# Kernel tuning notes

Measured on AMD Instinct MI355X. Metric: run time of the kernel, lower is better.

Reference implementation:

```python
import jax, jax.numpy as jnp
import numpy as np

L = 2048      # atoms
I = 512       # tokens (tok_idx.max()+1, fixed for jit)
C_ATOM = 128
C_PAIR = 16
C_TOK = 384
F1D = 3 + 1 + 128 + 256  # concat of atom 1d features = 388
NB, NH, HD = 3, 4, 32    # atom transformer blocks / heads / head dim
FF = 4 * C_ATOM


def _w(k, shape, fan_in):
    return jax.random.normal(k, shape, jnp.float32) / np.sqrt(fan_in)


def setup_inputs() -> dict:
    key = jax.random.key(0)
    ks = jax.random.split(key, 32)
    inp = {
        'ref_pos': jax.random.normal(ks[0], (L, 3), jnp.float32),
        'ref_charge': jax.random.normal(ks[1], (L, 1), jnp.float32),
        'ref_element': jax.random.uniform(ks[2], (L, 128), jnp.float32),
        'ref_atom_name_chars': jax.random.uniform(ks[3], (L, 256), jnp.float32),
        'ref_space_uid': jnp.sort(jax.random.randint(ks[4], (L,), 0, 64, jnp.int32)),
        'atom_to_token_map': jnp.sort(jax.random.randint(ks[5], (L,), 0, I, jnp.int32)),
        # linearNoBias weights stored (in, out)
        'W_in': _w(ks[6], (F1D, C_ATOM), F1D),
        'W_d': _w(ks[7], (3, C_PAIR), 3),
        'W_invd': _w(ks[8], (1, C_PAIR), 1),
        'W_vm': _w(ks[9], (1, C_PAIR), 1),
        'W_sl': _w(ks[10], (C_ATOM, C_PAIR), C_ATOM),
        'W_sm': _w(ks[11], (C_ATOM, C_PAIR), C_ATOM),
        'Wp1': _w(ks[12], (C_PAIR, C_PAIR), C_PAIR),
        'Wp2': _w(ks[13], (C_PAIR, C_PAIR), C_PAIR),
        'Wp3': _w(ks[14], (C_PAIR, C_PAIR), C_PAIR),
        'Wq_tok': _w(ks[15], (C_ATOM, C_TOK), C_ATOM),
        # atom transformer (stacked over NB blocks)
        'Wq': _w(ks[16], (NB, C_ATOM, C_ATOM), C_ATOM),
        'Wk': _w(ks[17], (NB, C_ATOM, C_ATOM), C_ATOM),
        'Wv': _w(ks[18], (NB, C_ATOM, C_ATOM), C_ATOM),
        'Wb': _w(ks[19], (NB, C_PAIR, NH), C_PAIR),
        'Wo': _w(ks[20], (NB, C_ATOM, C_ATOM), C_ATOM),
        'Wt1': _w(ks[21], (NB, C_ATOM, FF), C_ATOM),
        'Wt2': _w(ks[22], (NB, FF, C_ATOM), FF),
    }
    return inp


def _ln(x):
    mu = jnp.mean(x, axis=-1, keepdims=True)
    var = jnp.mean(jnp.square(x - mu), axis=-1, keepdims=True)
    return (x - mu) * jax.lax.rsqrt(var + 1e-5)


def _forward(ref_pos, ref_charge, ref_element, ref_atom_name_chars,
             ref_space_uid, atom_to_token_map,
             W_in, W_d, W_invd, W_vm, W_sl, W_sm, Wp1, Wp2, Wp3, Wq_tok,
             Wq, Wk, Wv, Wb, Wo, Wt1, Wt2):
    relu = jax.nn.relu
    # C_L: [L, c_atom]
    feat = jnp.concatenate([ref_pos, ref_charge, ref_element, ref_atom_name_chars], axis=-1)
    C_L = feat @ W_in
    # pairwise geometry: D_LL [L, L, 3], valid mask V_LL [L, L, 1]
    D = ref_pos[:, None, :] - ref_pos[None, :, :]
    Vf = (ref_space_uid[:, None] == ref_space_uid[None, :]).astype(C_L.dtype)[..., None]
    P = (D @ W_d) * Vf
    inv_d = 1.0 / (1.0 + jnp.linalg.norm(D, axis=-1, keepdims=True))
    P = P + (inv_d @ W_invd) * Vf
    P = P + (Vf @ W_vm) * Vf
    P = P + (relu(C_L) @ W_sl)[:, None, :] + (relu(C_L) @ W_sm)[None, :, :]
    P = P + relu(relu(relu(P) @ Wp1) @ Wp2) @ Wp3  # pair_mlp residual
    # atom transformer with pair bias
    Q = C_L
    scale = 1.0 / np.sqrt(HD)
    for b in range(NB):
        x = _ln(Q)
        q = (x @ Wq[b]).reshape(L, NH, HD)
        k = (x @ Wk[b]).reshape(L, NH, HD)
        v = (x @ Wv[b]).reshape(L, NH, HD)
        bias = P @ Wb[b]                                   # [L, L, NH]
        logits = jnp.einsum('lhd,mhd->lmh', q, k) * scale + bias
        a = jax.nn.softmax(logits, axis=1)                 # over keys m
        o = jnp.einsum('lmh,mhd->lhd', a, v).reshape(L, C_ATOM)
        Q = Q + o @ Wo[b]
        y = _ln(Q)
        Q = Q + relu(y @ Wt1[b]) @ Wt2[b]
    # process_q then scatter-mean (index_reduce 'mean', include_self=False)
    pQ = relu(Q @ Wq_tok)                                  # [L, c_token]
    tok = atom_to_token_map
    sums = jax.ops.segment_sum(pQ, tok, num_segments=I)
    cnt = jax.ops.segment_sum(jnp.ones((L, 1), pQ.dtype), tok, num_segments=I)
    A_I = sums / jnp.maximum(cnt, 1.0)
    return A_I, Q, C_L, P


def reference(ref_pos, ref_charge, ref_element, ref_atom_name_chars,
              ref_space_uid, atom_to_token_map,
              W_in, W_d, W_invd, W_vm, W_sl, W_sm, Wp1, Wp2, Wp3, Wq_tok,
              Wq, Wk, Wv, Wb, Wo, Wt1, Wt2):
    return _forward(ref_pos, ref_charge, ref_element, ref_atom_name_chars,
                    ref_space_uid, atom_to_token_map,
                    W_in, W_d, W_invd, W_vm, W_sl, W_sm, Wp1, Wp2, Wp3, Wq_tok,
                    Wq, Wk, Wv, Wb, Wo, Wt1, Wt2)
```

## Files before the change

kernel.cpp:

```cpp
#include <hip/hip_runtime.h>
#include <hip/hip_bf16.h>
#include <hip/hip_fp16.h>

#define L_ATOMS 2048
#define N_TOK 512
#define CA 128
#define CP 16
#define CT 384
#define NBLK 3
#define NHEAD 4
#define HDIM 32
#define FFD 512
#define F1D 388

typedef _Float16 half8 __attribute__((ext_vector_type(8)));
typedef _Float16 half4_t __attribute__((ext_vector_type(4)));
typedef float f32x4 __attribute__((ext_vector_type(4)));

__global__ __launch_bounds__(256) void k_cl(
    const float* __restrict__ pos, const float* __restrict__ charge,
    const float* __restrict__ elem, const float* __restrict__ chars,
    const float* __restrict__ W_in, const float* __restrict__ W_sl,
    const float* __restrict__ W_sm,
    float* __restrict__ out_cl, float* __restrict__ out_q,
    float* __restrict__ csl, float* __restrict__ csm) {
  __shared__ float feat_s[4][F1D];
  __shared__ float rcl_s[4][CA];
  const int t = threadIdx.x;
  const int l0 = blockIdx.x * 4;
  if (t < 12) feat_s[t / 3][t % 3] = pos[l0 * 3 + t];
  else if (t < 16) feat_s[t - 12][3] = charge[l0 + t - 12];
  for (int k = 0; k < 2; k++) {
    int idx = t + k * 256;
    feat_s[idx >> 7][4 + (idx & 127)] = elem[l0 * 128 + idx];
  }
  for (int k = 0; k < 4; k++) {
    int idx = t + k * 256;
    feat_s[idx >> 8][132 + (idx & 255)] = chars[l0 * 256 + idx];
  }
  __syncthreads();
  const int c = t & 127, rh = t >> 7;
  float acc[2] = {0.f, 0.f};
  for (int f4 = 0; f4 < F1D; f4 += 4) {
    float w0 = W_in[(f4 + 0) * CA + c];
    float w1 = W_in[(f4 + 1) * CA + c];
    float w2 = W_in[(f4 + 2) * CA + c];
    float w3 = W_in[(f4 + 3) * CA + c];
#pragma unroll
    for (int r = 0; r < 2; r++) {
      float4 fv = *(const float4*)&feat_s[rh * 2 + r][f4];
      acc[r] += fv.x * w0 + fv.y * w1 + fv.z * w2 + fv.w * w3;
    }
  }
#pragma unroll
  for (int r = 0; r < 2; r++) {
    int l = l0 + rh * 2 + r;
    out_cl[l * CA + c] = acc[r];
    out_q[l * CA + c] = acc[r];
    rcl_s[rh * 2 + r][c] = fmaxf(acc[r], 0.f);
  }
  __syncthreads();
  if (t < 128) {
    const int r = t >> 5, j = t & 15, mat = (t >> 4) & 1;
    const float* W = mat ? W_sm : W_sl;
    float a = 0.f;
    for (int i4 = 0; i4 < CA; i4 += 4) {
      float4 xv = *(const float4*)&rcl_s[r][i4];
      a += xv.x * W[i4 * CP + j] + xv.y * W[(i4 + 1) * CP + j] +
           xv.z * W[(i4 + 2) * CP + j] + xv.w * W[(i4 + 3) * CP + j];
    }
    float* dst = mat ? csm : csl;
    dst[(l0 + r) * CP + j] = a;
  }
}

__global__ __launch_bounds__(256, 4) void k_pair(
    const float* __restrict__ pos, const int* __restrict__ uid,
    const float* __restrict__ csl, const float* __restrict__ csm,
    const float* __restrict__ W_d, const float* __restrict__ W_invd,
    const float* __restrict__ W_vm, const float* __restrict__ Wp1,
    const float* __restrict__ Wp2, const float* __restrict__ Wp3,
    const float* __restrict__ Wb,
    float* __restrict__ P_out, _Float16* __restrict__ bias_hp, int use_bias) {
  __shared__ _Float16 bias_lds[12 * 2 * 256];
  const int t = threadIdx.x;
  const int w = t >> 6, lane = t & 63;
  const int q = lane >> 4, j16 = lane & 15;
  const int c4 = q * 4;
  const int m_base = blockIdx.x * 256;
  const int l0 = blockIdx.y * 2;
  half4_t w1f, w2f, w3f, wbf;
#pragma unroll
  for (int r = 0; r < 4; r++) {
    w1f[r] = (_Float16)Wp1[(c4 + r) * 16 + j16];
    w2f[r] = (_Float16)Wp2[(c4 + r) * 16 + j16];
    w3f[r] = (_Float16)Wp3[(c4 + r) * 16 + j16];
  }
  if (j16 < 12) {
    int bb = j16 >> 2, hh = j16 & 3;
#pragma unroll
    for (int r = 0; r < 4; r++)
      wbf[r] = (_Float16)Wb[(bb * 16 + c4 + r) * 4 + hh];
  } else {
    wbf = half4_t{0, 0, 0, 0};
  }
  const float4 wdx = *(const float4*)(W_d + c4);
  const float4 wdy = *(const float4*)(W_d + 16 + c4);
  const float4 wdz = *(const float4*)(W_d + 32 + c4);
  const float4 wiv = *(const float4*)(W_invd + c4);
  const float4 wvm = *(const float4*)(W_vm + c4);
  const float4 cl[2] = {*(const float4*)(csl + l0 * 16 + c4),
                        *(const float4*)(csl + (l0 + 1) * 16 + c4)};
  const float plx[2] = {pos[l0 * 3 + 0], pos[(l0 + 1) * 3 + 0]};
  const float ply[2] = {pos[l0 * 3 + 1], pos[(l0 + 1) * 3 + 1]};
  const float plz[2] = {pos[l0 * 3 + 2], pos[(l0 + 1) * 3 + 2]};
  const int uidl[2] = {uid[l0], uid[l0 + 1]};
  const f32x4 z = {0.f, 0.f, 0.f, 0.f};
#pragma unroll
  for (int it = 0; it < 4; it++) {
    const int moff = w * 64 + it * 16 + j16;
    const int m = m_base + moff;
    const float pmx = pos[m * 3 + 0], pmy = pos[m * 3 + 1],
                pmz = pos[m * 3 + 2];
    const int um = uid[m];
    const float4 cm = *(const float4*)(csm + m * 16 + c4);
#pragma unroll
    for (int li = 0; li < 2; li++) {
      const int lg = l0 + li;
      float dx = plx[li] - pmx, dy = ply[li] - pmy, dz = plz[li] - pmz;
      float vfm = (uidl[li] == um) ? 1.f : 0.f;
      float d2 = dx * dx + dy * dy + dz * dz;
      float invd_v =
          vfm * __builtin_amdgcn_rcpf(1.f + __builtin_amdgcn_sqrtf(d2));
      float dxv = dx * vfm, dyv = dy * vfm, dzv = dz * vfm;
      float pv[4];
      pv[0] = dxv * wdx.x + dyv * wdy.x + dzv * wdz.x + invd_v * wiv.x +
              vfm * wvm.x + cl[li].x + cm.x;
      pv[1] = dxv * wdx.y + dyv * wdy.y + dzv * wdz.y + invd_v * wiv.y +
              vfm * wvm.y + cl[li].y + cm.y;
      pv[2] = dxv * wdx.z + dyv * wdy.z + dzv * wdz.z + invd_v * wiv.z +
              vfm * wvm.z + cl[li].z + cm.z;
      pv[3] = dxv * wdx.w + dyv * wdy.w + dzv * wdz.w + invd_v * wiv.w +
              vfm * wvm.w + cl[li].w + cm.w;
      half4_t b0, b1, b2;
#pragma unroll
      for (int r = 0; r < 4; r++) b0[r] = (_Float16)fmaxf(pv[r], 0.f);
      f32x4 d = __builtin_amdgcn_mfma_f32_16x16x16f16(w1f, b0, z, 0, 0, 0);
#pragma unroll
      for (int r = 0; r < 4; r++) b1[r] = (_Float16)fmaxf(d[r], 0.f);
      d = __builtin_amdgcn_mfma_f32_16x16x16f16(w2f, b1, z, 0, 0, 0);
#pragma unroll
      for (int r = 0; r < 4; r++) b2[r] = (_Float16)fmaxf(d[r], 0.f);
      d = __builtin_amdgcn_mfma_f32_16x16x16f16(w3f, b2, z, 0, 0, 0);
      float pf[4];
#pragma unroll
      for (int r = 0; r < 4; r++) pf[r] = pv[r] + d[r];
      *(float4*)(P_out + ((size_t)lg * L_ATOMS + m) * 16 + c4) =
          make_float4(pf[0], pf[1], pf[2], pf[3]);
      if (use_bias) {
        half4_t bf;
#pragma unroll
        for (int r = 0; r < 4; r++) bf[r] = (_Float16)pf[r];
        f32x4 db = __builtin_amdgcn_mfma_f32_16x16x16f16(wbf, bf, z, 0, 0, 0);
        if (q < 3) {
#pragma unroll
          for (int r = 0; r < 4; r++)
            bias_lds[((q * 4 + r) * 2 + li) * 256 + moff] = (_Float16)db[r];
        }
      }
    }
  }
  if (use_bias) {
    __syncthreads();
    const size_t plane = (size_t)L_ATOMS * L_ATOMS;
#pragma unroll
    for (int kk = 0; kk < 3; kk++) {
      int cid = t + kk * 256;
      int pl = cid >> 6;
      int lrow = (cid >> 5) & 1;
      int chunk = cid & 31;
      half8 v = *(const half8*)&bias_lds[(pl * 2 + lrow) * 256 + chunk * 8];
      *(half8*)(bias_hp + pl * plane + (size_t)(l0 + lrow) * L_ATOMS + m_base +
                chunk * 8) = v;
    }
  }
}

__global__ __launch_bounds__(512, 4) void k_lnqkv(
    const float* __restrict__ Qg, const float* __restrict__ Wq,
    const float* __restrict__ Wk, const float* __restrict__ Wv,
    _Float16* __restrict__ q_hd, _Float16* __restrict__ k_hd,
    _Float16* __restrict__ vT_hd) {
  __shared__ float x_s[4][CA];
  const int t = threadIdx.x;
  const int l0 = blockIdx.x * 4;
  if (t < 128) ((float4*)x_s)[t] = ((const float4*)(Qg + l0 * CA))[t];
  __syncthreads();
  if (t < 128) {
    const int r = t >> 5, i = t & 31;
    float s1 = 0.f, s2 = 0.f;
#pragma unroll
    for (int k = 0; k < 4; k++) {
      float x = x_s[r][i + 32 * k];
      s1 += x;
      s2 += x * x;
    }
#pragma unroll
    for (int m = 1; m <= 16; m <<= 1) {
      s1 += __shfl_xor(s1, m);
      s2 += __shfl_xor(s2, m);
    }
    float mu = s1 * (1.f / 128.f);
    float var = s2 * (1.f / 128.f) - mu * mu;
    float inv = 1.f / sqrtf(var + 1e-5f);
#pragma unroll
    for (int k = 0; k < 4; k++)
      x_s[r][i + 32 * k] = (x_s[r][i + 32 * k] - mu) * inv;
  }
  __syncthreads();
  const int c = t & 127, rh = t >> 7;
  const int h = c >> 5, d = c & 31;
  const int l = l0 + rh;
#pragma unroll
  for (int mat = 0; mat < 3; mat++) {
    const float* W = mat == 0 ? Wq : (mat == 1 ? Wk : Wv);
    float acc = 0.f;
    for (int i4 = 0; i4 < CA; i4 += 4) {
      float w0 = W[(i4 + 0) * CA + c];
      float w1 = W[(i4 + 1) * CA + c];
      float w2 = W[(i4 + 2) * CA + c];
      float w3 = W[(i4 + 3) * CA + c];
      float4 xv = *(const float4*)&x_s[rh][i4];
      acc += xv.x * w0 + xv.y * w1 + xv.z * w2 + xv.w * w3;
    }
    if (mat == 0)
      q_hd[(h * L_ATOMS + l) * HDIM + d] = (_Float16)acc;
    else if (mat == 1)
      k_hd[(h * L_ATOMS + l) * HDIM + d] = (_Float16)acc;
    else
      vT_hd[(h * HDIM + d) * L_ATOMS + l] = (_Float16)acc;
  }
}

template <int USE_BIAS>
__global__ __launch_bounds__(512, 4) void k_attn(
    const _Float16* __restrict__ q_hd, const _Float16* __restrict__ k_hd,
    const _Float16* __restrict__ vT_hd, const _Float16* __restrict__ bias_hp,
    const float* __restrict__ Pmat, const float* __restrict__ Wb,
    float* __restrict__ o_buf, int b) {
  __shared__ __align__(16) _Float16 p_lds[8][16][40];
  __shared__ float o_sh[8][16][33];
  __shared__ float M_sh[8][16];
  __shared__ float S_sh[8][16];
  __shared__ float wb_s[16];
  const int t = threadIdx.x;
  const int w = t >> 6, lane = t & 63;
  const int l0 = blockIdx.x * 16;
  const int h = blockIdx.y;
  if (USE_BIAS == 0) {
    if (t < 16) wb_s[t] = Wb[(b * 16 + t) * 4 + h];
    __syncthreads();
  }
  const int c16 = lane & 15, q4 = lane >> 4;
  half8 qa = *(const half8*)(q_hd + ((h * L_ATOMS + l0 + c16) * HDIM + q4 * 8));
  f32x4 o0 = {0.f, 0.f, 0.f, 0.f}, o1 = {0.f, 0.f, 0.f, 0.f};
  float M = -INFINITY;
  float S = 0.f;
  const float scale = 0.17677669529663687f;
  const _Float16* bias_row =
      bias_hp + ((size_t)(b * 4 + h) * L_ATOMS + (l0 + c16)) * L_ATOMS;
  for (int it = 0; it < 8; it++) {
    const int m0 = w * 256 + it * 32;
    half8 kb0 =
        *(const half8*)(k_hd + ((h * L_ATOMS + m0 + c16) * HDIM + q4 * 8));
    half8 kb1 =
        *(const half8*)(k_hd + ((h * L_ATOMS + m0 + 16 + c16) * HDIM + q4 * 8));
    half8 vb0 =
        *(const half8*)(vT_hd + ((h * HDIM + c16) * L_ATOMS + m0 + q4 * 8));
    half8 vb1 = *(const half8*)(vT_hd +
                                ((h * HDIM + 16 + c16) * L_ATOMS + m0 + q4 * 8));
    f32x4 z = {0.f, 0.f, 0.f, 0.f};
    f32x4 c0 = __builtin_amdgcn_mfma_f32_16x16x32_f16(kb0, qa, z, 0, 0, 0);
    f32x4 c1 = __builtin_amdgcn_mfma_f32_16x16x32_f16(kb1, qa, z, 0, 0, 0);
    float l0v[4], l1v[4];
    if (USE_BIAS) {
      half4_t bh0 = *(const half4_t*)(bias_row + m0 + q4 * 4);
      half4_t bh1 = *(const half4_t*)(bias_row + m0 + 16 + q4 * 4);
#pragma unroll
      for (int r = 0; r < 4; r++) {
        l0v[r] = c0[r] * scale + (float)bh0[r];
        l1v[r] = c1[r] * scale + (float)bh1[r];
      }
    } else {
#pragma unroll
      for (int r = 0; r < 4; r++) {
        const float* Pp0 =
            Pmat + ((size_t)(l0 + c16) * L_ATOMS + m0 + q4 * 4 + r) * 16;
        const float* Pp1 = Pp0 + 16 * 16;
        float a0 = 0.f, a1 = 0.f;
#pragma unroll
        for (int c2 = 0; c2 < 16; c2++) {
          a0 += Pp0[c2] * wb_s[c2];
          a1 += Pp1[c2] * wb_s[c2];
        }
        l0v[r] = c0[r] * scale + a0;
        l1v[r] = c1[r] * scale + a1;
      }
    }
    float tm = fmaxf(fmaxf(fmaxf(l0v[0], l0v[1]), fmaxf(l0v[2], l0v[3])),
                     fmaxf(fmaxf(l1v[0], l1v[1]), fmaxf(l1v[2], l1v[3])));
    tm = fmaxf(tm, __shfl_xor(tm, 16));
    tm = fmaxf(tm, __shfl_xor(tm, 32));
    float Mn = fmaxf(M, tm);
    float al = __expf(M - Mn);
    float p0[4], p1[4], ps = 0.f;
#pragma unroll
    for (int r = 0; r < 4; r++) {
      p0[r] = __expf(l0v[r] - Mn);
      p1[r] = __expf(l1v[r] - Mn);
      ps += p0[r] + p1[r];
    }
    float rs = ps + __shfl_xor(ps, 16);
    rs += __shfl_xor(rs, 32);
    S = S * al + rs;
    M = Mn;
    half4_t ph0, ph1;
#pragma unroll
    for (int r = 0; r < 4; r++) {
      ph0[r] = (_Float16)p0[r];
      ph1[r] = (_Float16)p1[r];
    }
    *(half4_t*)&p_lds[w][c16][q4 * 4] = ph0;
    *(half4_t*)&p_lds[w][c16][16 + q4 * 4] = ph1;
    float alr[4];
#pragma unroll
    for (int r = 0; r < 4; r++) alr[r] = __shfl(al, q4 * 4 + r);
#pragma unroll
    for (int r = 0; r < 4; r++) {
      o0[r] *= alr[r];
      o1[r] *= alr[r];
    }
    asm volatile("" ::: "memory");
    __builtin_amdgcn_sched_barrier(0);
    half8 pa = *(const half8*)(&p_lds[w][c16][q4 * 8]);
    o0 = __builtin_amdgcn_mfma_f32_16x16x32_f16(pa, vb0, o0, 0, 0, 0);
    o1 = __builtin_amdgcn_mfma_f32_16x16x32_f16(pa, vb1, o1, 0, 0, 0);
    asm volatile("" ::: "memory");
    __builtin_amdgcn_sched_barrier(0);
  }
#pragma unroll
  for (int r = 0; r < 4; r++) {
    o_sh[w][q4 * 4 + r][c16] = o0[r];
    o_sh[w][q4 * 4 + r][16 + c16] = o1[r];
  }
  if (q4 == 0) {
    M_sh[w][c16] = M;
    S_sh[w][c16] = S;
  }
  __syncthreads();
  {
    const int d = t & 31, row = t >> 5;
    float Mg = M_sh[0][row];
#pragma unroll
    for (int ww = 1; ww < 8; ww++) Mg = fmaxf(Mg, M_sh[ww][row]);
    float Sg = 0.f, ov = 0.f;
#pragma unroll
    for (int ww = 0; ww < 8; ww++) {
      float e = __expf(M_sh[ww][row] - Mg);
      Sg += S_sh[ww][row] * e;
      ov += o_sh[ww][row][d] * e;
    }
    o_buf[(l0 + row) * CA + h * HDIM + d] = ov / Sg;
  }
}

__global__ __launch_bounds__(512, 4) void k_ffn(
    float* __restrict__ Qg, const float* __restrict__ o_buf,
    const float* __restrict__ Wo, const float* __restrict__ Wt1,
    const float* __restrict__ Wt2) {
  __shared__ float o_s[4][CA];
  __shared__ float q_s[4][CA];
  __shared__ float h_s[4][FFD];
  const int t = threadIdx.x;
  const int l0 = blockIdx.x * 4;
  if (t < 128) {
    ((float4*)o_s)[t] = ((const float4*)(o_buf + l0 * CA))[t];
    ((float4*)q_s)[t] = ((const float4*)(Qg + l0 * CA))[t];
  }
  __syncthreads();
  const int c = t & 127, rh = t >> 7;
  {
    float acc = 0.f;
    for (int i4 = 0; i4 < CA; i4 += 4) {
      float w0 = Wo[(i4 + 0) * CA + c];
      float w1 = Wo[(i4 + 1) * CA + c];
      float w2 = Wo[(i4 + 2) * CA + c];
      float w3 = Wo[(i4 + 3) * CA + c];
      float4 ov = *(const float4*)&o_s[rh][i4];
      acc += ov.x * w0 + ov.y * w1 + ov.z * w2 + ov.w * w3;
    }
    q_s[rh][c] += acc;
  }
  __syncthreads();
  if (t < 128) {
    const int r = t >> 5, i = t & 31;
    float s1 = 0.f, s2 = 0.f;
#pragma unroll
    for (int k = 0; k < 4; k++) {
      float x = q_s[r][i + 32 * k];
      s1 += x;
      s2 += x * x;
    }
#pragma unroll
    for (int m = 1; m <= 16; m <<= 1) {
      s1 += __shfl_xor(s1, m);
      s2 += __shfl_xor(s2, m);
    }
    float mu = s1 * (1.f / 128.f);
    float var = s2 * (1.f / 128.f) - mu * mu;
    float inv = 1.f / sqrtf(var + 1e-5f);
#pragma unroll
    for (int k = 0; k < 4; k++)
      o_s[r][i + 32 * k] = (q_s[r][i + 32 * k] - mu) * inv;
  }
  __syncthreads();
  {
    float a[4] = {0.f, 0.f, 0.f, 0.f};
    for (int i4 = 0; i4 < CA; i4 += 4) {
      float wv[4];
#pragma unroll
      for (int qq = 0; qq < 4; qq++) wv[qq] = Wt1[(i4 + qq) * FFD + t];
#pragma unroll
      for (int r = 0; r < 4; r++) {
        float4 yv = *(const float4*)&o_s[r][i4];
        a[r] += yv.x * wv[0] + yv.y * wv[1] + yv.z * wv[2] + yv.w * wv[3];
      }
    }
#pragma unroll
    for (int r = 0; r < 4; r++) h_s[r][t] = fmaxf(a[r], 0.f);
  }
  __syncthreads();
  {
    float acc = 0.f;
    for (int j4 = 0; j4 < FFD; j4 += 4) {
      float w0 = Wt2[(j4 + 0) * CA + c];
      float w1 = Wt2[(j4 + 1) * CA + c];
      float w2 = Wt2[(j4 + 2) * CA + c];
      float w3 = Wt2[(j4 + 3) * CA + c];
      float4 hv = *(const float4*)&h_s[rh][j4];
      acc += hv.x * w0 + hv.y * w1 + hv.z * w2 + hv.w * w3;
    }
    Qg[(l0 + rh) * CA + c] = q_s[rh][c] + acc;
  }
}

__global__ __launch_bounds__(256) void k_tok_mm(
    const float* __restrict__ Qg, const float* __restrict__ Wq_tok,
    float* __restrict__ pQ) {
  const int t = threadIdx.x;
  const int w = t >> 6, lane = t & 63;
  const int q = lane >> 4, j16 = lane & 15;
  const int c0 = blockIdx.x * 16;
  const int r0 = (blockIdx.y * 4 + w) * 16;
  f32x4 acc = {0.f, 0.f, 0.f, 0.f};
#pragma unroll
  for (int kk = 0; kk < 4; kk++) {
    const float* ap = Qg + (r0 + j16) * CA + kk * 32 + q * 8;
    float4 a0 = *(const float4*)ap;
    float4 a1 = *(const float4*)(ap + 4);
    half8 af = {(_Float16)a0.x, (_Float16)a0.y, (_Float16)a0.z, (_Float16)a0.w,
                (_Float16)a1.x, (_Float16)a1.y, (_Float16)a1.z, (_Float16)a1.w};
    half8 bf;
#pragma unroll
    for (int jj = 0; jj < 8; jj++)
      bf[jj] = (_Float16)Wq_tok[(kk * 32 + q * 8 + jj) * CT + c0 + j16];
    acc = __builtin_amdgcn_mfma_f32_16x16x32_f16(af, bf, acc, 0, 0, 0);
  }
#pragma unroll
  for (int r = 0; r < 4; r++)
    pQ[(r0 + q * 4 + r) * CT + c0 + j16] = fmaxf(acc[r], 0.f);
}

__global__ __launch_bounds__(384) void k_tok_mean(
    const float* __restrict__ pQ, const int* __restrict__ tok,
    float* __restrict__ A_I) {
  __shared__ int lo_s, hi_s;
  const int i = blockIdx.x;
  const int t = threadIdx.x;
  if (t == 0) {
    int lo = 0, hi = L_ATOMS;
    while (lo < hi) {
      int mid = (lo + hi) >> 1;
      if (tok[mid] < i) lo = mid + 1; else hi = mid;
    }
    lo_s = lo;
    int lo2 = lo, hi2 = L_ATOMS;
    while (lo2 < hi2) {
      int mid = (lo2 + hi2) >> 1;
      if (tok[mid] < i + 1) lo2 = mid + 1; else hi2 = mid;
    }
    hi_s = lo2;
  }
  __syncthreads();
  const int lo = lo_s, hi = hi_s;
  float acc = 0.f;
  for (int a = lo; a < hi; a++) acc += pQ[a * CT + t];
  int cnt = hi - lo;
  A_I[i * CT + t] = cnt > 0 ? acc / (float)cnt : 0.f;
}

extern "C" void kernel_launch(void* const* d_in, const int* in_sizes, int n_in,
                              void* d_out, int out_size, void* d_ws,
                              size_t ws_size, hipStream_t stream) {
  const float* pos = (const float*)d_in[0];
  const float* charge = (const float*)d_in[1];
  const float* elem = (const float*)d_in[2];
  const float* chars = (const float*)d_in[3];
  const int* uid = (const int*)d_in[4];
  const int* tok = (const int*)d_in[5];
  const float* W_in = (const float*)d_in[6];
  const float* W_d = (const float*)d_in[7];
  const float* W_invd = (const float*)d_in[8];
  const float* W_vm = (const float*)d_in[9];
  const float* W_sl = (const float*)d_in[10];
  const float* W_sm = (const float*)d_in[11];
  const float* Wp1 = (const float*)d_in[12];
  const float* Wp2 = (const float*)d_in[13];
  const float* Wp3 = (const float*)d_in[14];
  const float* Wq_tok = (const float*)d_in[15];
  const float* Wq = (const float*)d_in[16];
  const float* Wk = (const float*)d_in[17];
  const float* Wv = (const float*)d_in[18];
  const float* Wb = (const float*)d_in[19];
  const float* Wo = (const float*)d_in[20];
  const float* Wt1 = (const float*)d_in[21];
  const float* Wt2 = (const float*)d_in[22];

  float* out = (float*)d_out;
  float* A_I = out;
  float* Qg = out + 196608;
  float* C_Lo = out + 458752;
  float* P_out = out + 720896;

  char* ws = (char*)d_ws;
  float* csl = (float*)(ws + 0);
  float* csm = (float*)(ws + 131072);
  _Float16* q_hd = (_Float16*)(ws + 262144);
  _Float16* k_hd = (_Float16*)(ws + 262144 + 524288);
  _Float16* vT_hd = (_Float16*)(ws + 262144 + 2 * 524288);
  float* o_buf = (float*)(ws + 262144 + 3 * 524288);
  _Float16* bias_hp = (_Float16*)(ws + 262144 + 3 * 524288 + 1048576);
  float* pQ = (float*)(ws + 0);
  size_t need =
      262144 + 3 * 524288 + 1048576 + (size_t)NBLK * NHEAD * L_ATOMS * L_ATOMS * 2;
  int use_bias = (ws_size >= need) ? 1 : 0;

  k_cl<<<512, 256, 0, stream>>>(pos, charge, elem, chars, W_in, W_sl, W_sm,
                                C_Lo, Qg, csl, csm);
  k_pair<<<dim3(8, 1024), 256, 0, stream>>>(pos, uid, csl, csm, W_d, W_invd,
                                            W_vm, Wp1, Wp2, Wp3, Wb, P_out,
                                            bias_hp, use_bias);
  for (int b = 0; b < NBLK; b++) {
    k_lnqkv<<<512, 512, 0, stream>>>(Qg, Wq + b * 16384, Wk + b * 16384,
                                     Wv + b * 16384, q_hd, k_hd, vT_hd);
    if (use_bias)
      k_attn<1><<<dim3(128, 4), 512, 0, stream>>>(q_hd, k_hd, vT_hd, bias_hp,
                                                  P_out, Wb, o_buf, b);
    else
      k_attn<0><<<dim3(128, 4), 512, 0, stream>>>(q_hd, k_hd, vT_hd, bias_hp,
                                                  P_out, Wb, o_buf, b);
    k_ffn<<<512, 512, 0, stream>>>(Qg, o_buf, Wo + b * 16384, Wt1 + b * 65536,
                                   Wt2 + b * 65536);
  }
  k_tok_mm<<<dim3(24, 32), 256, 0, stream>>>(Qg, Wq_tok, pQ);
  k_tok_mean<<<512, 384, 0, stream>>>(pQ, tok, A_I);
}
```

Before: 650.8 us.

## Fuse LayerNorm+QKV projection into preceding kernels and skip trivial softmax rescale

Removes the standalone LN+QKV kernel. The first block's QKV is computed at the end of k_cl, and each later block's QKV is computed at the end of the previous block's FFN kernel, while the freshly updated Q rows are still in shared memory. This drops three kernel launches and a re-read of Q from global memory. The flash-attention loop also skips the shuffle and rescale of the output accumulators when no row max changed across the wavefront, which adds a wave-wide vote plus a branch in exchange.

```diff
diff --git a/kernel.cpp b/kernel.cpp
--- a/kernel.cpp
+++ b/kernel.cpp
@@ -21,11 +21,15 @@
     const float* __restrict__ pos, const float* __restrict__ charge,
     const float* __restrict__ elem, const float* __restrict__ chars,
     const float* __restrict__ W_in, const float* __restrict__ W_sl,
-    const float* __restrict__ W_sm,
+    const float* __restrict__ W_sm, const float* __restrict__ Wq,
+    const float* __restrict__ Wk, const float* __restrict__ Wv,
     float* __restrict__ out_cl, float* __restrict__ out_q,
-    float* __restrict__ csl, float* __restrict__ csm) {
+    float* __restrict__ csl, float* __restrict__ csm,
+    _Float16* __restrict__ q_hd, _Float16* __restrict__ k_hd,
+    _Float16* __restrict__ vT_hd) {
   __shared__ float feat_s[4][F1D];
   __shared__ float rcl_s[4][CA];
+  __shared__ float cl_s[4][CA];
   const int t = threadIdx.x;
   const int l0 = blockIdx.x * 4;
   if (t < 12) feat_s[t / 3][t % 3] = pos[l0 * 3 + t];
@@ -39,7 +43,7 @@
     feat_s[idx >> 8][132 + (idx & 255)] = chars[l0 * 256 + idx];
   }
   __syncthreads();
-  const int c = t & 127, rh = t >> 7;
+  const int c = t & 127, g = t >> 7;
   float acc[2] = {0.f, 0.f};
   for (int f4 = 0; f4 < F1D; f4 += 4) {
     float w0 = W_in[(f4 + 0) * CA + c];
@@ -48,16 +52,17 @@
     float w3 = W_in[(f4 + 3) * CA + c];
 #pragma unroll
     for (int r = 0; r < 2; r++) {
-      float4 fv = *(const float4*)&feat_s[rh * 2 + r][f4];
+      float4 fv = *(const float4*)&feat_s[g * 2 + r][f4];
       acc[r] += fv.x * w0 + fv.y * w1 + fv.z * w2 + fv.w * w3;
     }
   }
 #pragma unroll
   for (int r = 0; r < 2; r++) {
-    int l = l0 + rh * 2 + r;
+    int l = l0 + g * 2 + r;
     out_cl[l * CA + c] = acc[r];
     out_q[l * CA + c] = acc[r];
-    rcl_s[rh * 2 + r][c] = fmaxf(acc[r], 0.f);
+    rcl_s[g * 2 + r][c] = fmaxf(acc[r], 0.f);
+    cl_s[g * 2 + r][c] = acc[r];
   }
   __syncthreads();
   if (t < 128) {
@@ -71,6 +76,53 @@
     }
     float* dst = mat ? csm : csl;
     dst[(l0 + r) * CP + j] = a;
+    const int i = t & 31;
+    float s1 = 0.f, s2 = 0.f;
+#pragma unroll
+    for (int k = 0; k < 4; k++) {
+      float x = cl_s[r][i + 32 * k];
+      s1 += x;
+      s2 += x * x;
+    }
+#pragma unroll
+    for (int m = 1; m <= 16; m <<= 1) {
+      s1 += __shfl_xor(s1, m);
+      s2 += __shfl_xor(s2, m);
+    }
+    float mu = s1 * (1.f / 128.f);
+    float var = s2 * (1.f / 128.f) - mu * mu;
+    float inv = 1.f / sqrtf(var + 1e-5f);
+#pragma unroll
+    for (int k = 0; k < 4; k++)
+      cl_s[r][i + 32 * k] = (cl_s[r][i + 32 * k] - mu) * inv;
+  }
+  __syncthreads();
+  const int h = c >> 5, d = c & 31;
+#pragma unroll
+  for (int mat = 0; mat < 3; mat++) {
+    const float* W = mat == 0 ? Wq : (mat == 1 ? Wk : Wv);
+    float a0 = 0.f, a1 = 0.f;
+    for (int i4 = 0; i4 < CA; i4 += 4) {
+      float w0 = W[(i4 + 0) * CA + c];
+      float w1 = W[(i4 + 1) * CA + c];
+      float w2 = W[(i4 + 2) * CA + c];
+      float w3 = W[(i4 + 3) * CA + c];
+      float4 x0 = *(const float4*)&cl_s[g * 2][i4];
+      float4 x1 = *(const float4*)&cl_s[g * 2 + 1][i4];
+      a0 += x0.x * w0 + x0.y * w1 + x0.z * w2 + x0.w * w3;
+      a1 += x1.x * w0 + x1.y * w1 + x1.z * w2 + x1.w * w3;
+    }
+    int la = l0 + g * 2, lb = la + 1;
+    if (mat == 0) {
+      q_hd[(h * L_ATOMS + la) * HDIM + d] = (_Float16)a0;
+      q_hd[(h * L_ATOMS + lb) * HDIM + d] = (_Float16)a1;
+    } else if (mat == 1) {
+      k_hd[(h * L_ATOMS + la) * HDIM + d] = (_Float16)a0;
+      k_hd[(h * L_ATOMS + lb) * HDIM + d] = (_Float16)a1;
+    } else {
+      vT_hd[(h * HDIM + d) * L_ATOMS + la] = (_Float16)a0;
+      vT_hd[(h * HDIM + d) * L_ATOMS + lb] = (_Float16)a1;
+    }
   }
 }
 
@@ -183,62 +235,6 @@
       *(half8*)(bias_hp + pl * plane + (size_t)(l0 + lrow) * L_ATOMS + m_base +
                 chunk * 8) = v;
     }
-  }
-}
-
-__global__ __launch_bounds__(512, 4) void k_lnqkv(
-    const float* __restrict__ Qg, const float* __restrict__ Wq,
-    const float* __restrict__ Wk, const float* __restrict__ Wv,
-    _Float16* __restrict__ q_hd, _Float16* __restrict__ k_hd,
-    _Float16* __restrict__ vT_hd) {
-  __shared__ float x_s[4][CA];
-  const int t = threadIdx.x;
-  const int l0 = blockIdx.x * 4;
-  if (t < 128) ((float4*)x_s)[t] = ((const float4*)(Qg + l0 * CA))[t];
-  __syncthreads();
-  if (t < 128) {
-    const int r = t >> 5, i = t & 31;
-    float s1 = 0.f, s2 = 0.f;
-#pragma unroll
-    for (int k = 0; k < 4; k++) {
-      float x = x_s[r][i + 32 * k];
-      s1 += x;
-      s2 += x * x;
-    }
-#pragma unroll
-    for (int m = 1; m <= 16; m <<= 1) {
-      s1 += __shfl_xor(s1, m);
-      s2 += __shfl_xor(s2, m);
-    }
-    float mu = s1 * (1.f / 128.f);
-    float var = s2 * (1.f / 128.f) - mu * mu;
-    float inv = 1.f / sqrtf(var + 1e-5f);
-#pragma unroll
-    for (int k = 0; k < 4; k++)
-      x_s[r][i + 32 * k] = (x_s[r][i + 32 * k] - mu) * inv;
-  }
-  __syncthreads();
-  const int c = t & 127, rh = t >> 7;
-  const int h = c >> 5, d = c & 31;
-  const int l = l0 + rh;
-#pragma unroll
-  for (int mat = 0; mat < 3; mat++) {
-    const float* W = mat == 0 ? Wq : (mat == 1 ? Wk : Wv);
-    float acc = 0.f;
-    for (int i4 = 0; i4 < CA; i4 += 4) {
-      float w0 = W[(i4 + 0) * CA + c];
-      float w1 = W[(i4 + 1) * CA + c];
-      float w2 = W[(i4 + 2) * CA + c];
-      float w3 = W[(i4 + 3) * CA + c];
-      float4 xv = *(const float4*)&x_s[rh][i4];
-      acc += xv.x * w0 + xv.y * w1 + xv.z * w2 + xv.w * w3;
-    }
-    if (mat == 0)
-      q_hd[(h * L_ATOMS + l) * HDIM + d] = (_Float16)acc;
-    else if (mat == 1)
-      k_hd[(h * L_ATOMS + l) * HDIM + d] = (_Float16)acc;
-    else
-      vT_hd[(h * HDIM + d) * L_ATOMS + l] = (_Float16)acc;
   }
 }
 
@@ -332,13 +328,15 @@
     }
     *(half4_t*)&p_lds[w][c16][q4 * 4] = ph0;
     *(half4_t*)&p_lds[w][c16][16 + q4 * 4] = ph1;
-    float alr[4];
-#pragma unroll
-    for (int r = 0; r < 4; r++) alr[r] = __shfl(al, q4 * 4 + r);
-#pragma unroll
-    for (int r = 0; r < 4; r++) {
-      o0[r] *= alr[r];
-      o1[r] *= alr[r];
+    if (!__all(al >= 1.0f)) {
+      float alr[4];
+#pragma unroll
+      for (int r = 0; r < 4; r++) alr[r] = __shfl(al, q4 * 4 + r);
+#pragma unroll
+      for (int r = 0; r < 4; r++) {
+        o0[r] *= alr[r];
+        o1[r] *= alr[r];
+      }
     }
     asm volatile("" ::: "memory");
     __builtin_amdgcn_sched_barrier(0);
@@ -374,10 +372,14 @@
   }
 }
 
+template <int DO_QKV>
 __global__ __launch_bounds__(512, 4) void k_ffn(
     float* __restrict__ Qg, const float* __restrict__ o_buf,
     const float* __restrict__ Wo, const float* __restrict__ Wt1,
-    const float* __restrict__ Wt2) {
+    const float* __restrict__ Wt2, const float* __restrict__ Wq,
+    const float* __restrict__ Wk, const float* __restrict__ Wv,
+    _Float16* __restrict__ q_hd, _Float16* __restrict__ k_hd,
+    _Float16* __restrict__ vT_hd) {
   __shared__ float o_s[4][CA];
   __shared__ float q_s[4][CA];
   __shared__ float h_s[4][FFD];
@@ -450,7 +452,55 @@
       float4 hv = *(const float4*)&h_s[rh][j4];
       acc += hv.x * w0 + hv.y * w1 + hv.z * w2 + hv.w * w3;
     }
-    Qg[(l0 + rh) * CA + c] = q_s[rh][c] + acc;
+    float fin = q_s[rh][c] + acc;
+    Qg[(l0 + rh) * CA + c] = fin;
+    if (DO_QKV) q_s[rh][c] = fin;
+  }
+  if (DO_QKV) {
+    __syncthreads();
+    if (t < 128) {
+      const int r = t >> 5, i = t & 31;
+      float s1 = 0.f, s2 = 0.f;
+#pragma unroll
+      for (int k = 0; k < 4; k++) {
+        float x = q_s[r][i + 32 * k];
+        s1 += x;
+        s2 += x * x;
+      }
+#pragma unroll
+      for (int m = 1; m <= 16; m <<= 1) {
+        s1 += __shfl_xor(s1, m);
+        s2 += __shfl_xor(s2, m);
+      }
+      float mu = s1 * (1.f / 128.f);
+      float var = s2 * (1.f / 128.f) - mu * mu;
+      float inv = 1.f / sqrtf(var + 1e-5f);
+#pragma unroll
+      for (int k = 0; k < 4; k++)
+        o_s[r][i + 32 * k] = (q_s[r][i + 32 * k] - mu) * inv;
+    }
+    __syncthreads();
+    const int h = c >> 5, d = c & 31;
+    const int l = l0 + rh;
+#pragma unroll
+    for (int mat = 0; mat < 3; mat++) {
+      const float* W = mat == 0 ? Wq : (mat == 1 ? Wk : Wv);
+      float acc = 0.f;
+      for (int i4 = 0; i4 < CA; i4 += 4) {
+        float w0 = W[(i4 + 0) * CA + c];
+        float w1 = W[(i4 + 1) * CA + c];
+        float w2 = W[(i4 + 2) * CA + c];
+        float w3 = W[(i4 + 3) * CA + c];
+        float4 xv = *(const float4*)&o_s[rh][i4];
+        acc += xv.x * w0 + xv.y * w1 + xv.z * w2 + xv.w * w3;
+      }
+      if (mat == 0)
+        q_hd[(h * L_ATOMS + l) * HDIM + d] = (_Float16)acc;
+      else if (mat == 1)
+        k_hd[(h * L_ATOMS + l) * HDIM + d] = (_Float16)acc;
+      else
+        vT_hd[(h * HDIM + d) * L_ATOMS + l] = (_Float16)acc;
+    }
   }
 }
 
@@ -556,21 +606,30 @@
   int use_bias = (ws_size >= need) ? 1 : 0;
 
   k_cl<<<512, 256, 0, stream>>>(pos, charge, elem, chars, W_in, W_sl, W_sm,
-                                C_Lo, Qg, csl, csm);
+                                Wq, Wk, Wv, C_Lo, Qg, csl, csm, q_hd, k_hd,
+                                vT_hd);
   k_pair<<<dim3(8, 1024), 256, 0, stream>>>(pos, uid, csl, csm, W_d, W_invd,
                                             W_vm, Wp1, Wp2, Wp3, Wb, P_out,
                                             bias_hp, use_bias);
   for (int b = 0; b < NBLK; b++) {
-    k_lnqkv<<<512, 512, 0, stream>>>(Qg, Wq + b * 16384, Wk + b * 16384,
-                                     Wv + b * 16384, q_hd, k_hd, vT_hd);
     if (use_bias)
       k_attn<1><<<dim3(128, 4), 512, 0, stream>>>(q_hd, k_hd, vT_hd, bias_hp,
                                                   P_out, Wb, o_buf, b);
     else
       k_attn<0><<<dim3(128, 4), 512, 0, stream>>>(q_hd, k_hd, vT_hd, bias_hp,
                                                   P_out, Wb, o_buf, b);
-    k_ffn<<<512, 512, 0, stream>>>(Qg, o_buf, Wo + b * 16384, Wt1 + b * 65536,
-                                   Wt2 + b * 65536);
+    if (b < NBLK - 1)
+      k_ffn<1><<<512, 512, 0, stream>>>(Qg, o_buf, Wo + b * 16384,
+                                        Wt1 + b * 65536, Wt2 + b * 65536,
+                                        Wq + (b + 1) * 16384,
+                                        Wk + (b + 1) * 16384,
+                                        Wv + (b + 1) * 16384, q_hd, k_hd,
+                                        vT_hd);
+    else
+      k_ffn<0><<<512, 512, 0, stream>>>(Qg, o_buf, Wo + b * 16384,
+                                        Wt1 + b * 65536, Wt2 + b * 65536,
+                                        nullptr, nullptr, nullptr, q_hd, k_hd,
+                                        vT_hd);
   }
   k_tok_mm<<<dim3(24, 32), 256, 0, stream>>>(Qg, Wq_tok, pQ);
   k_tok_mean<<<512, 384, 0, stream>>>(pQ, tok, A_I);
```

Measured after the change: 685.1 us. +5.3%, slower.
